# Optimization experiments

Measured on AMD Instinct MI355X. Metric: run time of the kernel, lower is better.

## Reference

```python
import jax, jax.numpy as jnp
import numpy as np

B, T, N = 256, 512, 128
GO, EOS = 1, 2  # mead-baseline Offsets
NEG = -10000.0


def setup_inputs() -> dict:
    key = jax.random.key(0)
    k1, k2, k3 = jax.random.split(key, 3)
    unaries = jax.random.normal(k1, (B, T, N), dtype=jnp.float32)
    # constraint mask: True where transition is INVALID (masked to -1e4)
    cmask = jax.random.bernoulli(k2, 0.3, (1, N, N))
    trans = jax.nn.log_softmax(
        jnp.where(cmask, jnp.float32(NEG), jnp.float32(0.0)), axis=1
    )  # [1, N, N], matches buffer construction in __init__
    lengths = jax.random.randint(k3, (B,), T // 2, T + 1).astype(jnp.int64)
    lengths = lengths.at[0].set(T)  # ensure max(lengths) == T
    return {"unaries": unaries, "trans": trans, "lengths": lengths}


def _viterbi(probv, trans, lengths, start_idx, end_idx):
    # probv: [T, B, N] log-probs; trans: [1, N, N]; lengths: [B]
    seq_len, batch, n_tags = probv.shape
    trans0 = trans[0]  # [N(cur), N(prev)]
    lengths = lengths.astype(jnp.int32)

    alphas = jnp.full((batch, n_tags), NEG, probv.dtype).at[:, start_idx].set(0.0)
    alphas = jax.nn.log_softmax(alphas, axis=-1)

    def step(alphas, xs):
        unary_t, i = xs  # [B, N], scalar
        ntv = alphas[:, None, :] + trans0[None]          # [B, N_cur, N_prev]
        bp = jnp.argmax(ntv, axis=2)                     # backpointers [B, N]
        new_alphas = jnp.max(ntv, axis=2) + unary_t      # [B, N]
        alphas = jnp.where((i < lengths)[:, None], new_alphas, alphas)
        return alphas, bp

    alphas, bps = jax.lax.scan(step, alphas, (probv, jnp.arange(seq_len)))

    terminal = alphas + trans0[end_idx][None, :]         # [B, N]
    path_score = jnp.max(terminal, axis=1)               # [B]
    best_tag = jnp.argmax(terminal, axis=1)              # [B]

    rev_len = seq_len - lengths - 1

    def back(btid, xs):
        bp, i = xs  # bp: [B, N]
        new = jnp.take_along_axis(bp, btid[:, None], axis=1)[:, 0]
        btid = jnp.where(i > rev_len, new, btid)
        return btid, btid

    _, ys = jax.lax.scan(back, best_tag, (bps[::-1], jnp.arange(seq_len)))
    full = jnp.concatenate([best_tag[None], ys], axis=0)  # [T+1, B]
    best_path = full[:seq_len][::-1]                       # [T, B]

    seq_mask = jnp.arange(seq_len)[:, None] < lengths[None, :]  # [T, B]
    best_path = jnp.where(seq_mask, best_path, 0)
    return best_path, path_score


def reference(unaries, trans, lengths):
    # constrained branch of TaggerGreedyDecoder.forward (batch_first=True)
    probv = jax.nn.log_softmax(jnp.swapaxes(unaries, 0, 1), axis=-1)  # [T,B,N]
    preds_tb, scores = _viterbi(probv, trans, lengths, GO, EOS)
    return jnp.swapaxes(preds_tb, 0, 1), scores  # ([B,T], [B])
```

## Files before the change

kernel.cpp:

```cpp
#include <hip/hip_runtime.h>

#define BB 256
#define TT 512
#define NN 128
#define GO_IDX 1
#define EOS_IDX 2
#define TSPLIT 368
#define NEGV (-10000.0f)
#define ASLOT(x) ((x) + (((x) >> 5) << 2))

#define STEP_BARRIER() asm volatile("s_waitcnt lgkmcnt(0)\n\ts_barrier" ::: "memory")

__device__ __forceinline__ float dpp_xor1_f(float x) {
    return __int_as_float(__builtin_amdgcn_update_dpp(0, __float_as_int(x), 0xB1, 0xF, 0xF, true));
}
__device__ __forceinline__ float dpp_xor2_f(float x) {
    return __int_as_float(__builtin_amdgcn_update_dpp(0, __float_as_int(x), 0x4E, 0xF, 0xF, true));
}
__device__ __forceinline__ int dpp_xor1_i(int x) {
    return __builtin_amdgcn_update_dpp(0, x, 0xB1, 0xF, 0xF, true);
}
__device__ __forceinline__ int dpp_xor2_i(int x) {
    return __builtin_amdgcn_update_dpp(0, x, 0x4E, 0xF, 0xF, true);
}

template <int USE_WS>
__global__ __launch_bounds__(512) void viterbi_kernel(
    float* __restrict__ u,
    const float* __restrict__ trans,
    const int*   __restrict__ lengths_raw,
    float* __restrict__ out,
    unsigned char* __restrict__ ws)
{
    __shared__ unsigned char bps[(TSPLIT - 1) * NN];
    __shared__ __align__(16) float prob[2][16][NN];
    __shared__ __align__(16) float alpha[2][144];
    __shared__ float fin_v[2];
    __shared__ int   fin_i[2];

    const int tid  = threadIdx.x;
    const int b    = blockIdx.x;
    const int wave = tid >> 6;
    const int lane = tid & 63;
    const int q    = tid & 3;
    const int cur  = tid >> 2;
    const int hw   = tid >> 5;
    const int l32  = tid & 31;

    int len;
    {
        int probe = lengths_raw[1];
        len = (probe == 0) ? lengths_raw[2 * b] : lengths_raw[b];
    }

    float* pb = u + (size_t)b * TT * NN;
    const float4* pb4 = (const float4*)pb;
    unsigned char* spb = USE_WS ? (ws + (size_t)b * ((TT - TSPLIT) * NN)) : (unsigned char*)pb;

    float tr[32];
    {
        const float4* t4 = (const float4*)(trans + cur * NN + q * 32);
#pragma unroll
        for (int i = 0; i < 8; ++i) {
            float4 v = t4[i];
            tr[4*i+0] = v.x; tr[4*i+1] = v.y; tr[4*i+2] = v.z; tr[4*i+3] = v.w;
        }
    }

    if (tid < NN) alpha[0][ASLOT(tid)] = (tid == GO_IDX) ? 0.0f : NEGV;

    auto normrow = [&](float4 v, float* dstrow) {
        float m = fmaxf(fmaxf(v.x, v.y), fmaxf(v.z, v.w));
#pragma unroll
        for (int off = 16; off; off >>= 1) m = fmaxf(m, __shfl_xor(m, off, 64));
        float s = expf(v.x - m) + expf(v.y - m) + expf(v.z - m) + expf(v.w - m);
#pragma unroll
        for (int off = 16; off; off >>= 1) s += __shfl_xor(s, off, 64);
        float ls = logf(s);
        ((float4*)dstrow)[l32] =
            make_float4((v.x - m) - ls, (v.y - m) - ls, (v.z - m) - ls, (v.w - m) - ls);
    };

    float4 R = pb4[hw * 32 + l32];
    normrow(R, &prob[0][hw][0]);
    R = pb4[(16 + hw) * 32 + l32];
    __syncthreads();

    const int nG = (len + 15) >> 4;
    for (int g = 0; g < nG; ++g) {
        const int tb = g << 4;
        float Pg[16];
#pragma unroll
        for (int k2 = 0; k2 < 16; ++k2) Pg[k2] = prob[g & 1][k2][cur];
        normrow(R, &prob[(g + 1) & 1][hw][0]);
        {
            int rr = tb + 32 + hw;
            if (rr > TT - 1) rr = TT - 1;
            R = pb4[rr * 32 + l32];
        }
#pragma unroll 4
        for (int k = 0; k < 16; ++k) {
            const int t = tb + k;
            if (t < len) {
                const float* ra = alpha[t & 1];
                float*       wa = alpha[(t & 1) ^ 1];
                const float4* a4 = (const float4*)(ra + q * 36);
                float v[32];
#pragma unroll
                for (int i = 0; i < 8; ++i) {
                    float4 a = a4[i];
                    v[4*i+0] = a.x + tr[4*i+0];
                    v[4*i+1] = a.y + tr[4*i+1];
                    v[4*i+2] = a.z + tr[4*i+2];
                    v[4*i+3] = a.w + tr[4*i+3];
                }
                float m1[16]; int i1[16];
#pragma unroll
                for (int j = 0; j < 16; ++j) {
                    bool tk = v[2*j+1] > v[2*j];
                    m1[j] = tk ? v[2*j+1] : v[2*j];
                    i1[j] = tk ? 2*j+1 : 2*j;
                }
                float m2[8]; int i2[8];
#pragma unroll
                for (int j = 0; j < 8; ++j) {
                    bool tk = m1[2*j+1] > m1[2*j];
                    m2[j] = tk ? m1[2*j+1] : m1[2*j];
                    i2[j] = tk ? i1[2*j+1] : i1[2*j];
                }
                float m3[4]; int i3[4];
#pragma unroll
                for (int j = 0; j < 4; ++j) {
                    bool tk = m2[2*j+1] > m2[2*j];
                    m3[j] = tk ? m2[2*j+1] : m2[2*j];
                    i3[j] = tk ? i2[2*j+1] : i2[2*j];
                }
                float m4[2]; int i4[2];
#pragma unroll
                for (int j = 0; j < 2; ++j) {
                    bool tk = m3[2*j+1] > m3[2*j];
                    m4[j] = tk ? m3[2*j+1] : m3[2*j];
                    i4[j] = tk ? i3[2*j+1] : i3[2*j];
                }
                bool tk5 = m4[1] > m4[0];
                float best = tk5 ? m4[1] : m4[0];
                int   bp   = (tk5 ? i4[1] : i4[0]) + q * 32;

                float v1 = dpp_xor1_f(best); int b1 = dpp_xor1_i(bp);
                bool  t1 = (q & 1) ? (v1 >= best) : (v1 > best);
                float mm1 = t1 ? v1 : best;  int p1 = t1 ? b1 : bp;
                float v2 = dpp_xor2_f(mm1);  int b2 = dpp_xor2_i(p1);
                bool  t2 = (q & 2) ? (v2 >= mm1) : (v2 > mm1);
                float M  = t2 ? v2 : mm1;    int BP = t2 ? b2 : p1;

                if (q == 0) {
                    wa[ASLOT(cur)] = M + Pg[k];
                    if (t >= 1) {
                        if (t < TSPLIT) bps[(t - 1) * NN + cur] = (unsigned char)BP;
                        else if (USE_WS) spb[(t - TSPLIT) * NN + cur] = (unsigned char)BP;
                        else             spb[(size_t)t * 512 + cur] = (unsigned char)BP;
                    }
                }
                STEP_BARRIER();
            }
        }
    }

    __threadfence();

    if (tid < NN) {
        float v = alpha[len & 1][ASLOT(tid)] + trans[EOS_IDX * NN + tid];
        int idx = tid;
#pragma unroll
        for (int off = 32; off; off >>= 1) {
            float ov = __shfl_xor(v, off, 64);
            int   oi = __shfl_xor(idx, off, 64);
            if (ov > v || (ov == v && oi < idx)) { v = ov; idx = oi; }
        }
        if (lane == 0) { fin_v[wave] = v; fin_i[wave] = idx; }
    }
    __syncthreads();

    const int lenU = __builtin_amdgcn_readfirstlane(len);

    for (int t = lenU + tid; t < TT; t += 512) out[(size_t)b * TT + t] = 0.0f;

    {
        unsigned int* cache = (unsigned int*)&prob[0][0][0];
        const volatile unsigned int* src = (const volatile unsigned int*)spb;
        for (int i = tid; i < 128 * 32; i += 512) {
            if (USE_WS) cache[i] = src[(size_t)(i >> 5) * 32 + (i & 31)];
            else        cache[i] = src[(size_t)(TSPLIT + (i >> 5)) * 128 + (i & 31)];
        }
    }
    __syncthreads();

    float sc; int T0;
    {
        float v0 = fin_v[0], v1 = fin_v[1];
        int   i0 = fin_i[0], i1 = fin_i[1];
        if (v1 > v0) { sc = v1; T0 = i1; }
        else         { sc = v0; T0 = i0; }
    }
    if (tid == 0) {
        out[(size_t)BB * TT + b] = sc;
        out[(size_t)b * TT + (lenU - 1)] = (float)T0;
    }

    const unsigned char* cacheb = (const unsigned char*)&prob[0][0][0];
    unsigned char* lt   = (unsigned char*)&alpha[0][0];
    unsigned char* Harr = lt + 1024;

    const int s  = wave;
    const int A  = lenU - 1 - 64 * s;
    const int h0 = lane;
    const int h1 = 64 + lane;
    const int Jmax = (A < 64) ? A : 64;

    unsigned int rec0[16], rec1[16];
#pragma unroll
    for (int i = 0; i < 16; ++i) { rec0[i] = 0u; rec1[i] = 0u; }

    int c0 = h0, c1 = h1;
#pragma unroll
    for (int j = 1; j <= 64; ++j) {
        if (j <= Jmax) {
            const int x = A - j + 1;
            int n0, n1;
            if (x < TSPLIT) {
                n0 = bps[(x - 1) * NN + c0];
                n1 = bps[(x - 1) * NN + c1];
            } else if (x < TSPLIT + 128) {
                n0 = cacheb[(x - TSPLIT) * NN + c0];
                n1 = cacheb[(x - TSPLIT) * NN + c1];
            } else {
                if (USE_WS) {
                    n0 = ((const volatile unsigned char*)spb)[(size_t)(x - TSPLIT) * NN + c0];
                    n1 = ((const volatile unsigned char*)spb)[(size_t)(x - TSPLIT) * NN + c1];
                } else {
                    n0 = ((const volatile unsigned char*)spb)[(size_t)x * 512 + c0];
                    n1 = ((const volatile unsigned char*)spb)[(size_t)x * 512 + c1];
                }
            }
            c0 = n0; c1 = n1;
            rec0[(j - 1) >> 2] |= (unsigned int)c0 << (((j - 1) & 3) * 8);
            rec1[(j - 1) >> 2] |= (unsigned int)c1 << (((j - 1) & 3) * 8);
        }
    }
    if (A >= 65) {
        lt[s * NN + h0] = (unsigned char)c0;
        lt[s * NN + h1] = (unsigned char)c1;
    }
    __syncthreads();

    if (tid == 0) {
        int H = T0;
        Harr[0] = (unsigned char)H;
#pragma unroll
        for (int ss = 1; ss < 8; ++ss) {
            if (lenU - 1 - 64 * ss >= 1) {
                H = lt[(ss - 1) * NN + H];
                Harr[ss] = (unsigned char)H;
            }
        }
    }
    __syncthreads();

    if (A >= 1) {
        const int Hs = Harr[s];
        if (h0 == Hs) {
#pragma unroll
            for (int j = 1; j <= 64; ++j)
                if (j <= Jmax)
                    out[(size_t)b * TT + (A - j)] =
                        (float)((rec0[(j - 1) >> 2] >> (((j - 1) & 3) * 8)) & 255u);
        }
        if (h1 == Hs) {
#pragma unroll
            for (int j = 1; j <= 64; ++j)
                if (j <= Jmax)
                    out[(size_t)b * TT + (A - j)] =
                        (float)((rec1[(j - 1) >> 2] >> (((j - 1) & 3) * 8)) & 255u);
        }
    }
}

extern "C" void kernel_launch(void* const* d_in, const int* in_sizes, int n_in,
                              void* d_out, int out_size, void* d_ws, size_t ws_size,
                              hipStream_t stream) {
    float*       unaries = (float*)d_in[0];
    const float* trans   = (const float*)d_in[1];
    const int*   lengths = (const int*)d_in[2];
    float* out = (float*)d_out;
    unsigned char* ws = (unsigned char*)d_ws;

    const size_t need = (size_t)BB * (TT - TSPLIT) * NN;
    if (ws != nullptr && ws_size >= need) {
        hipLaunchKernelGGL(HIP_KERNEL_NAME(viterbi_kernel<1>), dim3(BB), dim3(512), 0, stream,
                           unaries, trans, lengths, out, ws);
    } else {
        hipLaunchKernelGGL(HIP_KERNEL_NAME(viterbi_kernel<0>), dim3(BB), dim3(512), 0, stream,
                           unaries, trans, lengths, out, ws);
    }
}
```

Before: 462.3 us.

## Defer backpointer argmax off the serial Viterbi critical path

Each Viterbi step now computes only the max with fmaxf and DPP reductions, so the next alpha is produced sooner. The argmax and backpointer store for step t are recomputed from saved candidate values during step t+1, after that step's alpha loads are issued, and a final flush runs after the loop. This shortens the per-step dependency chain before the barrier, at the cost of keeping 32 extra floats live in registers and some duplicated compare work. If the compiler does not overlap the shadow argmax with the loads and barrier, register pressure could offset the gain.

```diff
diff --git a/kernel.cpp b/kernel.cpp
--- a/kernel.cpp
+++ b/kernel.cpp
@@ -81,6 +81,56 @@
             make_float4((v.x - m) - ls, (v.y - m) - ls, (v.z - m) - ls, (v.w - m) - ls);
     };
 
+    float cv[32];
+    int   c_t = 0;
+
+    auto bp_shadow = [&](int ct) {
+        float m1[16]; int i1[16];
+#pragma unroll
+        for (int j = 0; j < 16; ++j) {
+            bool tk = cv[2*j+1] > cv[2*j];
+            m1[j] = tk ? cv[2*j+1] : cv[2*j];
+            i1[j] = tk ? 2*j+1 : 2*j;
+        }
+        float m2[8]; int i2[8];
+#pragma unroll
+        for (int j = 0; j < 8; ++j) {
+            bool tk = m1[2*j+1] > m1[2*j];
+            m2[j] = tk ? m1[2*j+1] : m1[2*j];
+            i2[j] = tk ? i1[2*j+1] : i1[2*j];
+        }
+        float m3[4]; int i3[4];
+#pragma unroll
+        for (int j = 0; j < 4; ++j) {
+            bool tk = m2[2*j+1] > m2[2*j];
+            m3[j] = tk ? m2[2*j+1] : m2[2*j];
+            i3[j] = tk ? i2[2*j+1] : i2[2*j];
+        }
+        float m4[2]; int i4[2];
+#pragma unroll
+        for (int j = 0; j < 2; ++j) {
+            bool tk = m3[2*j+1] > m3[2*j];
+            m4[j] = tk ? m3[2*j+1] : m3[2*j];
+            i4[j] = tk ? i3[2*j+1] : i3[2*j];
+        }
+        bool tk5 = m4[1] > m4[0];
+        float best = tk5 ? m4[1] : m4[0];
+        int   bp   = (tk5 ? i4[1] : i4[0]) + q * 32;
+
+        float v1 = dpp_xor1_f(best); int b1 = dpp_xor1_i(bp);
+        bool  t1 = (q & 1) ? (v1 >= best) : (v1 > best);
+        float mm1 = t1 ? v1 : best;  int p1 = t1 ? b1 : bp;
+        float v2 = dpp_xor2_f(mm1);  int b2 = dpp_xor2_i(p1);
+        bool  t2 = (q & 2) ? (v2 >= mm1) : (v2 > mm1);
+        int BP = t2 ? b2 : p1;
+
+        if (q == 0 && ct >= 1) {
+            if (ct < TSPLIT) bps[(ct - 1) * NN + cur] = (unsigned char)BP;
+            else if (USE_WS) spb[(ct - TSPLIT) * NN + cur] = (unsigned char)BP;
+            else             spb[(size_t)ct * 512 + cur] = (unsigned char)BP;
+        }
+    };
+
     float4 R = pb4[hw * 32 + l32];
     normrow(R, &prob[0][hw][0]);
     R = pb4[(16 + hw) * 32 + l32];
@@ -105,66 +155,36 @@
                 const float* ra = alpha[t & 1];
                 float*       wa = alpha[(t & 1) ^ 1];
                 const float4* a4 = (const float4*)(ra + q * 36);
-                float v[32];
+                float4 av[8];
+#pragma unroll
+                for (int i = 0; i < 8; ++i) av[i] = a4[i];
+                if (t > 0) bp_shadow(c_t);
 #pragma unroll
                 for (int i = 0; i < 8; ++i) {
-                    float4 a = a4[i];
-                    v[4*i+0] = a.x + tr[4*i+0];
-                    v[4*i+1] = a.y + tr[4*i+1];
-                    v[4*i+2] = a.z + tr[4*i+2];
-                    v[4*i+3] = a.w + tr[4*i+3];
+                    cv[4*i+0] = av[i].x + tr[4*i+0];
+                    cv[4*i+1] = av[i].y + tr[4*i+1];
+                    cv[4*i+2] = av[i].z + tr[4*i+2];
+                    cv[4*i+3] = av[i].w + tr[4*i+3];
                 }
-                float m1[16]; int i1[16];
-#pragma unroll
-                for (int j = 0; j < 16; ++j) {
-                    bool tk = v[2*j+1] > v[2*j];
-                    m1[j] = tk ? v[2*j+1] : v[2*j];
-                    i1[j] = tk ? 2*j+1 : 2*j;
-                }
-                float m2[8]; int i2[8];
-#pragma unroll
-                for (int j = 0; j < 8; ++j) {
-                    bool tk = m1[2*j+1] > m1[2*j];
-                    m2[j] = tk ? m1[2*j+1] : m1[2*j];
-                    i2[j] = tk ? i1[2*j+1] : i1[2*j];
-                }
-                float m3[4]; int i3[4];
-#pragma unroll
-                for (int j = 0; j < 4; ++j) {
-                    bool tk = m2[2*j+1] > m2[2*j];
-                    m3[j] = tk ? m2[2*j+1] : m2[2*j];
-                    i3[j] = tk ? i2[2*j+1] : i2[2*j];
-                }
-                float m4[2]; int i4[2];
-#pragma unroll
-                for (int j = 0; j < 2; ++j) {
-                    bool tk = m3[2*j+1] > m3[2*j];
-                    m4[j] = tk ? m3[2*j+1] : m3[2*j];
-                    i4[j] = tk ? i3[2*j+1] : i3[2*j];
-                }
-                bool tk5 = m4[1] > m4[0];
-                float best = tk5 ? m4[1] : m4[0];
-                int   bp   = (tk5 ? i4[1] : i4[0]) + q * 32;
-
-                float v1 = dpp_xor1_f(best); int b1 = dpp_xor1_i(bp);
-                bool  t1 = (q & 1) ? (v1 >= best) : (v1 > best);
-                float mm1 = t1 ? v1 : best;  int p1 = t1 ? b1 : bp;
-                float v2 = dpp_xor2_f(mm1);  int b2 = dpp_xor2_i(p1);
-                bool  t2 = (q & 2) ? (v2 >= mm1) : (v2 > mm1);
-                float M  = t2 ? v2 : mm1;    int BP = t2 ? b2 : p1;
-
-                if (q == 0) {
-                    wa[ASLOT(cur)] = M + Pg[k];
-                    if (t >= 1) {
-                        if (t < TSPLIT) bps[(t - 1) * NN + cur] = (unsigned char)BP;
-                        else if (USE_WS) spb[(t - TSPLIT) * NN + cur] = (unsigned char)BP;
-                        else             spb[(size_t)t * 512 + cur] = (unsigned char)BP;
-                    }
-                }
+                float w0[16];
+#pragma unroll
+                for (int j = 0; j < 16; ++j) w0[j] = fmaxf(cv[2*j], cv[2*j+1]);
+                float w1[4];
+#pragma unroll
+                for (int j = 0; j < 4; ++j)
+                    w1[j] = fmaxf(fmaxf(w0[4*j], w0[4*j+1]), fmaxf(w0[4*j+2], w0[4*j+3]));
+                float best = fmaxf(fmaxf(w1[0], w1[1]), fmaxf(w1[2], w1[3]));
+                float mq = fmaxf(best, dpp_xor1_f(best));
+                float M  = fmaxf(mq, dpp_xor2_f(mq));
+
+                if (q == 0) wa[ASLOT(cur)] = M + Pg[k];
+                c_t = t;
                 STEP_BARRIER();
             }
         }
     }
+
+    bp_shadow(c_t);
 
     __threadfence();
 
```

Result: slower. 486.4 us (+5.2%).
